# Performance work log

Hardware: AMD Instinct MI355X
Metric: run time of the kernel (lower is better)

## Reference

```python
import jax, jax.numpy as jnp
import numpy as np

DIM = 512
BLOCK = 64
SPARSITY = 0.9
B, L = 4, 2048
NEG_INF = jnp.float32(-jnp.inf)


def _block_sparse_mask(key, seq_len, block_size, sparsity):
    # mirrors BasicQuantumAttention._get_block_sparse_mask, with diagonal
    # blocks forced on so no softmax row is fully masked (avoids NaNs)
    nb = (seq_len + block_size - 1) // block_size
    blk = jax.random.uniform(key, (nb, nb)) > sparsity
    blk = jnp.tril(blk) | jnp.eye(nb, dtype=bool)
    m = jnp.repeat(jnp.repeat(blk, block_size, axis=0), block_size, axis=1)
    return m[:seq_len, :seq_len]


def setup_inputs() -> dict:
    key = jax.random.key(0)
    ks = jax.random.split(key, 12)
    d = DIM
    inp = {}
    names = ['q_real', 'q_imag', 'k_real', 'k_imag', 'v_real', 'v_imag']
    for i, n in enumerate(names):
        inp[n] = jax.random.normal(ks[i], (B, L, d), dtype=jnp.float32)
    # xavier-ish init for Linear weights (torch Linear: y = x @ W.T + b)
    s6 = (2.0 / (6 * d + 6 * d)) ** 0.5
    s2 = (2.0 / (2 * d + 2 * d)) ** 0.5
    inp['W_qkv'] = jax.random.normal(ks[6], (6 * d, 6 * d), dtype=jnp.float32) * s6
    inp['b_qkv'] = jnp.zeros((6 * d,), dtype=jnp.float32)
    inp['W_out'] = jax.random.normal(ks[7], (2 * d, 2 * d), dtype=jnp.float32) * s2
    inp['b_out'] = jnp.zeros((2 * d,), dtype=jnp.float32)
    # two independent random block-sparse masks (one per stream, as in the
    # original which regenerates the mask inside each _chunk_attention call)
    inp['mask_real'] = _block_sparse_mask(ks[8], L, BLOCK, SPARSITY)
    inp['mask_imag'] = _block_sparse_mask(ks[9], L, BLOCK, SPARSITY)
    return inp


def _masked_attention(q, k, v, mask, scale):
    # q,k,v: [B,L,d]; mask: [L,L] bool (True = keep)
    scores = jnp.einsum('bqd,bkd->bqk', q, k) * scale
    scores = jnp.where(mask[None, :, :], scores, NEG_INF)
    attn = jax.nn.softmax(scores, axis=-1)  # dropout is identity in eval
    return jnp.einsum('bqk,bkd->bqd', attn, v)


def reference(q_real, q_imag, k_real, k_imag, v_real, v_imag,
              W_qkv, b_qkv, W_out, b_out, mask_real, mask_imag):
    d = q_real.shape[-1]
    scale = jnp.asarray(d, q_real.dtype) ** -0.5
    x = jnp.concatenate([q_real, q_imag, k_real, k_imag, v_real, v_imag], axis=-1)
    qkv = x @ W_qkv.T + b_qkv                       # [B,L,6d]
    q_r, q_i, k_r, k_i, v_r, v_i = jnp.split(qkv, 6, axis=-1)
    out_real = _masked_attention(q_r, k_r, v_r, mask_real, scale)
    out_imag = _masked_attention(q_i, k_i, v_i, mask_imag, scale)
    out = jnp.concatenate([out_real, out_imag], axis=-1)  # [B,L,2d]
    out = out @ W_out.T + b_out
    return out[..., :d], out[..., d:]
```

## Files before the change

### kernel.cpp

```cpp
#include <hip/hip_runtime.h>
#include <stdint.h>

typedef __attribute__((ext_vector_type(8))) short short8;
typedef __attribute__((ext_vector_type(4))) float f32x4;

#define DEV __device__ __forceinline__

DEV unsigned short f2bf(float f) {
    unsigned int u = __float_as_uint(f);
    u += 0x7FFFu + ((u >> 16) & 1u);
    return (unsigned short)(u >> 16);
}

DEV void gload_lds16(const void* g, void* l) {
    __builtin_amdgcn_global_load_lds(
        (const __attribute__((address_space(1))) unsigned int*)g,
        (__attribute__((address_space(3))) unsigned int*)l,
        16, 0, 0);
}

__global__ __launch_bounds__(256) void f32_to_bf16_k(
    const float* __restrict__ in, unsigned short* __restrict__ out, int n8) {
    int i = blockIdx.x * 256 + threadIdx.x;
    if (i >= n8) return;
    const float4* src = (const float4*)in + (size_t)i * 2;
    float4 a = src[0], b = src[1];
    short8 o;
    o[0] = f2bf(a.x); o[1] = f2bf(a.y); o[2] = f2bf(a.z); o[3] = f2bf(a.w);
    o[4] = f2bf(b.x); o[5] = f2bf(b.y); o[6] = f2bf(b.z); o[7] = f2bf(b.w);
    *((short8*)out + i) = o;
}

__global__ __launch_bounds__(256) void pack_x_k(
    const float* __restrict__ p0, const float* __restrict__ p1,
    const float* __restrict__ p2, const float* __restrict__ p3,
    const float* __restrict__ p4, const float* __restrict__ p5,
    unsigned short* __restrict__ x) {
    int i = blockIdx.x * 256 + threadIdx.x;
    int e0 = i * 8;
    int m = e0 / 3072;
    int k = e0 - m * 3072;
    int sel = k >> 9;
    const float* src;
    switch (sel) {
        case 0: src = p0; break; case 1: src = p1; break;
        case 2: src = p2; break; case 3: src = p3; break;
        case 4: src = p4; break; default: src = p5; break;
    }
    src += (size_t)m * 512 + (k & 511);
    float4 a = *(const float4*)src;
    float4 b = *(const float4*)(src + 4);
    short8 o;
    o[0] = f2bf(a.x); o[1] = f2bf(a.y); o[2] = f2bf(a.z); o[3] = f2bf(a.w);
    o[4] = f2bf(b.x); o[5] = f2bf(b.y); o[6] = f2bf(b.z); o[7] = f2bf(b.w);
    *(short8*)(x + e0) = o;
}

__global__ void scan_masks_k(const void* mr, const void* mi,
                             int* __restrict__ nact, unsigned char* __restrict__ lists) {
    int t = threadIdx.x;
    if (t >= 64) return;
    int s = t >> 5, qb = t & 31;
    const unsigned char* det = (const unsigned char*)mr;
    bool is_byte = det[1] != 0;
    const void* m = s ? mi : mr;
    int cnt = 0;
    for (int kb = 0; kb < 32; ++kb) {
        size_t off = (size_t)(qb * 64) * 2048 + (size_t)kb * 64;
        bool on = is_byte ? (((const unsigned char*)m)[off] != 0)
                          : (((const int*)m)[off] != 0);
        if (on) lists[t * 32 + cnt++] = (unsigned char)kb;
    }
    nact[t] = cnt;
}


#define MFMA16(mbase)                                                          \
    do {                                                                       \
        _Pragma("unroll")                                                      \
        for (int m_ = 0; m_ < 4; ++m_) {                                       \
            _Pragma("unroll")                                                  \
            for (int n_ = 0; n_ < 4; ++n_)                                     \
                acc[(mbase) + m_][n_] = __builtin_amdgcn_mfma_f32_16x16x32_bf16( \
                    af[m_], bf[n_], acc[(mbase) + m_][n_], 0, 0, 0);           \
        }                                                                      \
    } while (0)

#define PHASE_PRE()                                          \
    __builtin_amdgcn_s_barrier();                            \
    asm volatile("s_waitcnt lgkmcnt(0)" ::: "memory");       \
    __builtin_amdgcn_sched_barrier(0);                       \
    __builtin_amdgcn_s_setprio(1)

#define PHASE_END()                                          \
    __builtin_amdgcn_s_setprio(0);                           \
    __builtin_amdgcn_s_barrier();                            \
    asm volatile("" ::: "memory")

#define PHASE_END_V4()                                       \
    __builtin_amdgcn_s_setprio(0);                           \
    asm volatile("s_waitcnt vmcnt(4)" ::: "memory");         \
    __builtin_amdgcn_s_barrier();                            \
    asm volatile("" ::: "memory")

template <int MODE>
__global__ __launch_bounds__(512, 2) void gemm256(
    const unsigned short* __restrict__ A, const unsigned short* __restrict__ B,
    const float* __restrict__ bias, unsigned short* __restrict__ Cb,
    float* __restrict__ Cf, int M, int N, int K, int NBN, int halfN, int half_elems) {
    __shared__ unsigned short lds[2][4][8192];
    const int tid = threadIdx.x;
    const int wv = tid >> 6, ln = tid & 63;
    const int fr = ln & 15, fo = ln >> 4;
    const int wr = wv >> 2, wc = wv & 3;
    const int cpx = gridDim.x >> 3;
    const int wgid = (blockIdx.x & 7) * cpx + (blockIdx.x >> 3);
    const int bm = wgid / NBN, bn = wgid % NBN;
    const unsigned short* Abase = A + (size_t)(bm * 256) * K;
    const unsigned short* Bbase = B + (size_t)(bn * 256) * K;
    const int NT = K >> 6;
    const int NI = NT >> 1;

    auto stagePair = [&](int buf, int isB, int t) {
        const unsigned short* G = isB ? Bbase : Abase;
        unsigned short* Ld = &lds[buf][isB ? 2 : 0][0];
        const int kcol = t * 64;
        #pragma unroll
        for (int r2 = 0; r2 < 4; ++r2) {
            int d = r2 * 8192 + wv * 1024 + ln * 16;
            int s = d ^ (((d >> 7) & 7) << 4);
            int grow = s >> 7;
            int gcol = (s & 127) >> 1;
            gload_lds16(G + (size_t)grow * K + kcol + gcol,
                        (char*)Ld + r2 * 8192 + wv * 1024);
        }
    };
    auto readA = [&](int buf, int mh, int ks, short8* dst) {
        #pragma unroll
        for (int m = 0; m < 4; ++m) {
            int row = wr * 128 + mh * 64 + m * 16 + fr;
            int byte = (row * 128 + ks * 64 + fo * 16) ^ ((row & 7) << 4);
            dst[m] = *(const short8*)((const char*)&lds[buf][0][0] + byte);
        }
    };
    auto readB = [&](int buf, int ks, short8* dst) {
        #pragma unroll
        for (int n = 0; n < 4; ++n) {
            int row = wc * 64 + n * 16 + fr;
            int byte = (row * 128 + ks * 64 + fo * 16) ^ ((row & 7) << 4);
            dst[n] = *(const short8*)((const char*)&lds[buf][2][0] + byte);
        }
    };

    f32x4 acc[8][4];
    #pragma unroll
    for (int m = 0; m < 8; ++m)
        #pragma unroll
        for (int n = 0; n < 4; ++n) acc[m][n] = f32x4{0.f, 0.f, 0.f, 0.f};

    stagePair(0, 0, 0);
    stagePair(0, 1, 0);
    stagePair(1, 1, 1);
    asm volatile("s_waitcnt vmcnt(4)" ::: "memory");
    __builtin_amdgcn_s_barrier();
    asm volatile("" ::: "memory");

    for (int i = 0; i < NI; ++i) {
        const int t1 = 2 * i + 1;
        const int tn0 = (2 * i + 2) % NT;
        const int tn1 = (2 * i + 3) % NT;
        short8 af[4], bf[4];
        readA(0, 0, 0, af); readB(0, 0, bf);
        stagePair(1, 0, t1);
        PHASE_PRE(); MFMA16(0); PHASE_END();
        readA(0, 1, 0, af);
        PHASE_PRE(); MFMA16(4); PHASE_END();
        readA(0, 0, 1, af); readB(0, 1, bf);
        PHASE_PRE(); MFMA16(0); PHASE_END();
        readA(0, 1, 1, af);
        stagePair(0, 1, tn0);
        PHASE_PRE(); MFMA16(4); PHASE_END_V4();
        readA(1, 0, 0, af); readB(1, 0, bf);
        stagePair(0, 0, tn0);
        PHASE_PRE(); MFMA16(0); PHASE_END();
        readA(1, 1, 0, af);
        PHASE_PRE(); MFMA16(4); PHASE_END();
        readA(1, 0, 1, af); readB(1, 1, bf);
        PHASE_PRE(); MFMA16(0); PHASE_END();
        readA(1, 1, 1, af);
        stagePair(1, 1, tn1);
        PHASE_PRE(); MFMA16(4); PHASE_END_V4();
    }

    #pragma unroll
    for (int mi = 0; mi < 8; ++mi)
        #pragma unroll
        for (int ni = 0; ni < 4; ++ni)
            #pragma unroll
            for (int j = 0; j < 4; ++j) {
                int gr = bm * 256 + wr * 128 + mi * 16 + fo * 4 + j;
                int gc = bn * 256 + wc * 64 + ni * 16 + fr;
                float v = acc[mi][ni][j] + bias[gc];
                if (MODE == 0) {
                    Cb[(size_t)gr * N + gc] = f2bf(v);
                } else {
                    if (gc < halfN) Cf[(size_t)gr * halfN + gc] = v;
                    else Cf[half_elems + (size_t)gr * halfN + (gc - halfN)] = v;
                }
            }
}

__global__ __launch_bounds__(256) void transpose_v_k(
    const unsigned short* __restrict__ qkv, unsigned short* __restrict__ Vt) {
    int idx = blockIdx.x;
    int kt = idx & 31; idx >>= 5;
    int dt = idx & 7;  idx >>= 3;
    int b  = idx & 3;  idx >>= 2;
    int s  = idx;
    __shared__ unsigned short tile[64][65];
    int t = threadIdx.x;
    int r = t >> 2;
    int cs = (t & 3) * 16;
    const unsigned short* src =
        qkv + (size_t)(b * 2048 + kt * 64 + r) * 3072 + 2048 + s * 512 + dt * 64 + cs;
    short8 v0 = *(const short8*)src;
    short8 v1 = *(const short8*)(src + 8);
    #pragma unroll
    for (int i = 0; i < 8; ++i) { tile[r][cs + i] = v0[i]; tile[r][cs + 8 + i] = v1[i]; }
    __syncthreads();
    short8 o0, o1;
    #pragma unroll
    for (int i = 0; i < 8; ++i) { o0[i] = tile[cs + i][r]; o1[i] = tile[cs + 8 + i][r]; }
    unsigned short* dst =
        Vt + (size_t)((s * 4 + b) * 512 + dt * 64 + r) * 2048 + kt * 64 + cs;
    *(short8*)dst = o0;
    *(short8*)(dst + 8) = o1;
}

__global__ __launch_bounds__(64) void attn_k(
    const unsigned short* __restrict__ qkv, const unsigned short* __restrict__ Vt,
    unsigned short* __restrict__ attn, const int* __restrict__ nact,
    const unsigned char* __restrict__ lists) {
    int wg = blockIdx.x;
    int xcd = wg & 7, idx = wg >> 3;
    int b = xcd >> 1, s = xcd & 1;
    int qb = idx >> 2, quarter = idx & 3;
    int lane = threadIdx.x;
    int fr = lane & 15, fo = lane >> 4;
    const float scale = 0.04419417382415922f;
    __shared__ unsigned short Pl[1024];
    unsigned char* Plb = (unsigned char*)&Pl[0];

    int qoff = s * 512, koff = 1024 + s * 512;
    size_t vtbase = (size_t)((s * 4 + b) * 512) * 2048;
    int mrow = b * 2048 + qb * 64 + quarter * 16;

    short8 qf[16];
    const unsigned short* qrow_ptr = qkv + (size_t)(mrow + fr) * 3072 + qoff + fo * 8;
    #pragma unroll
    for (int kk = 0; kk < 16; ++kk) qf[kk] = *(const short8*)(qrow_ptr + kk * 32);

    f32x4 acc[32];
    #pragma unroll
    for (int di = 0; di < 32; ++di) acc[di] = f32x4{0.f, 0.f, 0.f, 0.f};
    float mr[4] = {-1e30f, -1e30f, -1e30f, -1e30f};
    float lr[4] = {0.f, 0.f, 0.f, 0.f};

    int na = nact[s * 32 + qb];
    const unsigned char* lst = lists + (s * 32 + qb) * 32;

    for (int t = 0; t < na; ++t) {
        int kb = lst[t];
        const unsigned short* kbase_ptr =
            qkv + (size_t)(b * 2048 + kb * 64 + fr) * 3072 + koff + fo * 8;
        f32x4 sf[4];
        #pragma unroll
        for (int nf = 0; nf < 4; ++nf) {
            sf[nf] = f32x4{0.f, 0.f, 0.f, 0.f};
            const unsigned short* kp = kbase_ptr + (size_t)nf * 16 * 3072;
            #pragma unroll
            for (int kk = 0; kk < 16; ++kk) {
                short8 kf = *(const short8*)(kp + kk * 32);
                sf[nf] = __builtin_amdgcn_mfma_f32_16x16x32_bf16(qf[kk], kf, sf[nf], 0, 0, 0);
            }
        }
        #pragma unroll
        for (int nf = 0; nf < 4; ++nf) sf[nf] *= scale;
        float bm[4], f_[4], rs[4];
        #pragma unroll
        for (int j = 0; j < 4; ++j) {
            float v = fmaxf(fmaxf(sf[0][j], sf[1][j]), fmaxf(sf[2][j], sf[3][j]));
            #pragma unroll
            for (int off = 1; off < 16; off <<= 1) v = fmaxf(v, __shfl_xor(v, off, 64));
            bm[j] = v;
        }
        #pragma unroll
        for (int j = 0; j < 4; ++j) {
            float mn = fmaxf(mr[j], bm[j]);
            f_[j] = __expf(mr[j] - mn);
            mr[j] = mn;
            rs[j] = 0.f;
        }
        #pragma unroll
        for (int nf = 0; nf < 4; ++nf)
            #pragma unroll
            for (int j = 0; j < 4; ++j) {
                float p = __expf(sf[nf][j] - mr[j]);
                sf[nf][j] = p;
                rs[j] += p;
            }
        #pragma unroll
        for (int j = 0; j < 4; ++j) {
            float v = rs[j];
            #pragma unroll
            for (int off = 1; off < 16; off <<= 1) v += __shfl_xor(v, off, 64);
            lr[j] = lr[j] * f_[j] + v;
        }
        #pragma unroll
        for (int di = 0; di < 32; ++di) {
            acc[di][0] *= f_[0]; acc[di][1] *= f_[1];
            acc[di][2] *= f_[2]; acc[di][3] *= f_[3];
        }
        #pragma unroll
        for (int nf = 0; nf < 4; ++nf)
            #pragma unroll
            for (int j = 0; j < 4; ++j) {
                int row = fo * 4 + j, col = nf * 16 + fr;
                int byte = row * 128 + ((col * 2) ^ ((row & 7) << 4));
                *(unsigned short*)(Plb + byte) = f2bf(sf[nf][j]);
            }
        asm volatile("s_waitcnt lgkmcnt(0)" ::: "memory");
        #pragma unroll
        for (int ks = 0; ks < 2; ++ks) {
            int rbyte = fr * 128 + (((ks * 32 + fo * 8) * 2) ^ ((fr & 7) << 4));
            short8 pf = *(const short8*)(Plb + rbyte);
            const unsigned short* vp =
                Vt + vtbase + (size_t)fr * 2048 + kb * 64 + ks * 32 + fo * 8;
            #pragma unroll
            for (int di = 0; di < 32; ++di) {
                short8 vf = *(const short8*)(vp + (size_t)di * 16 * 2048);
                acc[di] = __builtin_amdgcn_mfma_f32_16x16x32_bf16(pf, vf, acc[di], 0, 0, 0);
            }
        }
    }
    float inv[4];
    #pragma unroll
    for (int j = 0; j < 4; ++j) inv[j] = 1.0f / lr[j];
    unsigned short* orow = attn + (size_t)(mrow + fo * 4) * 1024 + s * 512 + fr;
    #pragma unroll
    for (int di = 0; di < 32; ++di)
        #pragma unroll
        for (int j = 0; j < 4; ++j)
            orow[(size_t)j * 1024 + di * 16] = f2bf(acc[di][j] * inv[j]);
}

extern "C" void kernel_launch(void* const* d_in, const int* in_sizes, int n_in,
                              void* d_out, int out_size, void* d_ws, size_t ws_size,
                              hipStream_t stream) {
    const float* q_r = (const float*)d_in[0];
    const float* q_i = (const float*)d_in[1];
    const float* k_r = (const float*)d_in[2];
    const float* k_i = (const float*)d_in[3];
    const float* v_r = (const float*)d_in[4];
    const float* v_i = (const float*)d_in[5];
    const float* W_qkv = (const float*)d_in[6];
    const float* b_qkv = (const float*)d_in[7];
    const float* W_out = (const float*)d_in[8];
    const float* b_out = (const float*)d_in[9];
    const void* mask_r = d_in[10];
    const void* mask_i = d_in[11];

    char* ws = (char*)d_ws;
    unsigned short* x    = (unsigned short*)(ws);
    unsigned short* Wq   = (unsigned short*)(ws + 50331648);
    unsigned short* qkv  = (unsigned short*)(ws + 69206016);
    unsigned short* Wo   = (unsigned short*)(ws + 119537664);
    int* nact            = (int*)(ws + 121634816);
    unsigned char* lists = (unsigned char*)(ws + 121634816 + 256);
    unsigned short* Vt   = x;
    unsigned short* attn = x + 8388608;

    f32_to_bf16_k<<<4608, 256, 0, stream>>>(W_qkv, Wq, 1179648);
    f32_to_bf16_k<<<512, 256, 0, stream>>>(W_out, Wo, 131072);
    pack_x_k<<<12288, 256, 0, stream>>>(q_r, q_i, k_r, k_i, v_r, v_i, x);
    scan_masks_k<<<1, 64, 0, stream>>>(mask_r, mask_i, nact, lists);
    gemm256<0><<<384, 512, 0, stream>>>(x, Wq, b_qkv, qkv, nullptr,
                                        8192, 3072, 3072, 12, 0, 0);
    transpose_v_k<<<2048, 256, 0, stream>>>(qkv, Vt);
    attn_k<<<1024, 64, 0, stream>>>(qkv, Vt, attn, nact, lists);
    gemm256<1><<<128, 512, 0, stream>>>(attn, Wo, b_out, nullptr, (float*)d_out,
                                        8192, 1024, 1024, 4, 512, 4194304);
}
```

Baseline: 531.4 us.

## Retile QKV GEMM to 256x192, split attention head dim, parallelize mask scan

The QKV projection GEMM is templated on the N-tile width and launched with 256x192 tiles, giving 512 workgroups instead of 384 for a better fit to the CU count. The attention kernel splits the 512-wide head dimension into two halves per workgroup, doubling the grid to 2048 and halving accumulator registers so two waves can fit per SIMD. The cost is that QK^T is recomputed once per half. The mask scan now uses one block per query block with a ballot and popcount compaction instead of a single serial thread loop, and the K-fragment loads are interleaved across the four score tiles.

```diff
diff --git a/kernel.cpp b/kernel.cpp
--- a/kernel.cpp
+++ b/kernel.cpp
@@ -58,29 +58,33 @@
 
 __global__ void scan_masks_k(const void* mr, const void* mi,
                              int* __restrict__ nact, unsigned char* __restrict__ lists) {
-    int t = threadIdx.x;
-    if (t >= 64) return;
-    int s = t >> 5, qb = t & 31;
+    int blk = blockIdx.x;
+    int s = blk >> 5, qb = blk & 31;
+    int lane = threadIdx.x;
     const unsigned char* det = (const unsigned char*)mr;
     bool is_byte = det[1] != 0;
     const void* m = s ? mi : mr;
-    int cnt = 0;
-    for (int kb = 0; kb < 32; ++kb) {
-        size_t off = (size_t)(qb * 64) * 2048 + (size_t)kb * 64;
-        bool on = is_byte ? (((const unsigned char*)m)[off] != 0)
-                          : (((const int*)m)[off] != 0);
-        if (on) lists[t * 32 + cnt++] = (unsigned char)kb;
+    bool on = false;
+    if (lane < 32) {
+        size_t off = (size_t)(qb * 64) * 2048 + (size_t)lane * 64;
+        on = is_byte ? (((const unsigned char*)m)[off] != 0)
+                     : (((const int*)m)[off] != 0);
     }
-    nact[t] = cnt;
-}
-
-
-#define MFMA16(mbase)                                                          \
+    unsigned long long mask = __ballot(on);
+    if (on) {
+        int pos = __popcll(mask & ((1ull << lane) - 1ull));
+        lists[blk * 32 + pos] = (unsigned char)lane;
+    }
+    if (lane == 0) nact[blk] = (int)__popcll(mask);
+}
+
+
+#define MFMA_TILE(mbase)                                                       \
     do {                                                                       \
         _Pragma("unroll")                                                      \
         for (int m_ = 0; m_ < 4; ++m_) {                                       \
             _Pragma("unroll")                                                  \
-            for (int n_ = 0; n_ < 4; ++n_)                                     \
+            for (int n_ = 0; n_ < NF; ++n_)                                    \
                 acc[(mbase) + m_][n_] = __builtin_amdgcn_mfma_f32_16x16x32_bf16( \
                     af[m_], bf[n_], acc[(mbase) + m_][n_], 0, 0, 0);           \
         }                                                                      \
@@ -97,18 +101,25 @@
     __builtin_amdgcn_s_barrier();                            \
     asm volatile("" ::: "memory")
 
-#define PHASE_END_V4()                                       \
+#define WAIT_VN()                                                          \
+    do {                                                                   \
+        if constexpr (NF == 3) asm volatile("s_waitcnt vmcnt(3)" ::: "memory"); \
+        else asm volatile("s_waitcnt vmcnt(4)" ::: "memory");              \
+    } while (0)
+
+#define PHASE_END_VN()                                       \
     __builtin_amdgcn_s_setprio(0);                           \
-    asm volatile("s_waitcnt vmcnt(4)" ::: "memory");         \
+    WAIT_VN();                                               \
     __builtin_amdgcn_s_barrier();                            \
     asm volatile("" ::: "memory")
 
-template <int MODE>
+template <int MODE, int NF>
 __global__ __launch_bounds__(512, 2) void gemm256(
     const unsigned short* __restrict__ A, const unsigned short* __restrict__ B,
     const float* __restrict__ bias, unsigned short* __restrict__ Cb,
     float* __restrict__ Cf, int M, int N, int K, int NBN, int halfN, int half_elems) {
-    __shared__ unsigned short lds[2][4][8192];
+    constexpr int BN = NF * 64;
+    __shared__ unsigned short lds[2][16384 + NF * 4096];
     const int tid = threadIdx.x;
     const int wv = tid >> 6, ln = tid & 63;
     const int fr = ln & 15, fo = ln >> 4;
@@ -117,20 +128,21 @@
     const int wgid = (blockIdx.x & 7) * cpx + (blockIdx.x >> 3);
     const int bm = wgid / NBN, bn = wgid % NBN;
     const unsigned short* Abase = A + (size_t)(bm * 256) * K;
-    const unsigned short* Bbase = B + (size_t)(bn * 256) * K;
+    const unsigned short* Bbase = B + (size_t)(bn * BN) * K;
     const int NT = K >> 6;
     const int NI = NT >> 1;
 
     auto stagePair = [&](int buf, int isB, int t) {
         const unsigned short* G = isB ? Bbase : Abase;
-        unsigned short* Ld = &lds[buf][isB ? 2 : 0][0];
+        unsigned short* Ld = &lds[buf][isB ? 16384 : 0];
         const int kcol = t * 64;
-        #pragma unroll
-        for (int r2 = 0; r2 < 4; ++r2) {
+        const int nch = isB ? NF : 4;
+        #pragma unroll
+        for (int r2 = 0; r2 < nch; ++r2) {
             int d = r2 * 8192 + wv * 1024 + ln * 16;
-            int s = d ^ (((d >> 7) & 7) << 4);
-            int grow = s >> 7;
-            int gcol = (s & 127) >> 1;
+            int sw = d ^ (((d >> 7) & 7) << 4);
+            int grow = sw >> 7;
+            int gcol = (sw & 127) >> 1;
             gload_lds16(G + (size_t)grow * K + kcol + gcol,
                         (char*)Ld + r2 * 8192 + wv * 1024);
         }
@@ -140,28 +152,28 @@
         for (int m = 0; m < 4; ++m) {
             int row = wr * 128 + mh * 64 + m * 16 + fr;
             int byte = (row * 128 + ks * 64 + fo * 16) ^ ((row & 7) << 4);
-            dst[m] = *(const short8*)((const char*)&lds[buf][0][0] + byte);
+            dst[m] = *(const short8*)((const char*)&lds[buf][0] + byte);
         }
     };
     auto readB = [&](int buf, int ks, short8* dst) {
         #pragma unroll
-        for (int n = 0; n < 4; ++n) {
-            int row = wc * 64 + n * 16 + fr;
+        for (int n = 0; n < NF; ++n) {
+            int row = wc * (NF * 16) + n * 16 + fr;
             int byte = (row * 128 + ks * 64 + fo * 16) ^ ((row & 7) << 4);
-            dst[n] = *(const short8*)((const char*)&lds[buf][2][0] + byte);
+            dst[n] = *(const short8*)((const char*)&lds[buf][16384] + byte);
         }
     };
 
-    f32x4 acc[8][4];
+    f32x4 acc[8][NF];
     #pragma unroll
     for (int m = 0; m < 8; ++m)
         #pragma unroll
-        for (int n = 0; n < 4; ++n) acc[m][n] = f32x4{0.f, 0.f, 0.f, 0.f};
+        for (int n = 0; n < NF; ++n) acc[m][n] = f32x4{0.f, 0.f, 0.f, 0.f};
 
     stagePair(0, 0, 0);
     stagePair(0, 1, 0);
     stagePair(1, 1, 1);
-    asm volatile("s_waitcnt vmcnt(4)" ::: "memory");
+    WAIT_VN();
     __builtin_amdgcn_s_barrier();
     asm volatile("" ::: "memory");
 
@@ -172,34 +184,34 @@
         short8 af[4], bf[4];
         readA(0, 0, 0, af); readB(0, 0, bf);
         stagePair(1, 0, t1);
-        PHASE_PRE(); MFMA16(0); PHASE_END();
+        PHASE_PRE(); MFMA_TILE(0); PHASE_END();
         readA(0, 1, 0, af);
-        PHASE_PRE(); MFMA16(4); PHASE_END();
+        PHASE_PRE(); MFMA_TILE(4); PHASE_END();
         readA(0, 0, 1, af); readB(0, 1, bf);
-        PHASE_PRE(); MFMA16(0); PHASE_END();
+        PHASE_PRE(); MFMA_TILE(0); PHASE_END();
         readA(0, 1, 1, af);
         stagePair(0, 1, tn0);
-        PHASE_PRE(); MFMA16(4); PHASE_END_V4();
+        PHASE_PRE(); MFMA_TILE(4); PHASE_END_VN();
         readA(1, 0, 0, af); readB(1, 0, bf);
         stagePair(0, 0, tn0);
-        PHASE_PRE(); MFMA16(0); PHASE_END();
+        PHASE_PRE(); MFMA_TILE(0); PHASE_END();
         readA(1, 1, 0, af);
-        PHASE_PRE(); MFMA16(4); PHASE_END();
+        PHASE_PRE(); MFMA_TILE(4); PHASE_END();
         readA(1, 0, 1, af); readB(1, 1, bf);
-        PHASE_PRE(); MFMA16(0); PHASE_END();
+        PHASE_PRE(); MFMA_TILE(0); PHASE_END();
         readA(1, 1, 1, af);
         stagePair(1, 1, tn1);
-        PHASE_PRE(); MFMA16(4); PHASE_END_V4();
+        PHASE_PRE(); MFMA_TILE(4); PHASE_END_VN();
     }
 
     #pragma unroll
     for (int mi = 0; mi < 8; ++mi)
         #pragma unroll
-        for (int ni = 0; ni < 4; ++ni)
+        for (int ni = 0; ni < NF; ++ni)
             #pragma unroll
             for (int j = 0; j < 4; ++j) {
                 int gr = bm * 256 + wr * 128 + mi * 16 + fo * 4 + j;
-                int gc = bn * 256 + wc * 64 + ni * 16 + fr;
+                int gc = bn * BN + wc * (NF * 16) + ni * 16 + fr;
                 float v = acc[mi][ni][j] + bias[gc];
                 if (MODE == 0) {
                     Cb[(size_t)gr * N + gc] = f2bf(v);
@@ -237,14 +249,14 @@
     *(short8*)(dst + 8) = o1;
 }
 
-__global__ __launch_bounds__(64) void attn_k(
+__global__ __launch_bounds__(64, 2) void attn_k(
     const unsigned short* __restrict__ qkv, const unsigned short* __restrict__ Vt,
     unsigned short* __restrict__ attn, const int* __restrict__ nact,
     const unsigned char* __restrict__ lists) {
     int wg = blockIdx.x;
     int xcd = wg & 7, idx = wg >> 3;
     int b = xcd >> 1, s = xcd & 1;
-    int qb = idx >> 2, quarter = idx & 3;
+    int qb = idx >> 3, quarter = (idx >> 1) & 3, dh = idx & 1;
     int lane = threadIdx.x;
     int fr = lane & 15, fo = lane >> 4;
     const float scale = 0.04419417382415922f;
@@ -252,7 +264,7 @@
     unsigned char* Plb = (unsigned char*)&Pl[0];
 
     int qoff = s * 512, koff = 1024 + s * 512;
-    size_t vtbase = (size_t)((s * 4 + b) * 512) * 2048;
+    size_t vtbase = (size_t)((s * 4 + b) * 512 + dh * 256) * 2048;
     int mrow = b * 2048 + qb * 64 + quarter * 16;
 
     short8 qf[16];
@@ -260,9 +272,9 @@
     #pragma unroll
     for (int kk = 0; kk < 16; ++kk) qf[kk] = *(const short8*)(qrow_ptr + kk * 32);
 
-    f32x4 acc[32];
-    #pragma unroll
-    for (int di = 0; di < 32; ++di) acc[di] = f32x4{0.f, 0.f, 0.f, 0.f};
+    f32x4 acc[16];
+    #pragma unroll
+    for (int di = 0; di < 16; ++di) acc[di] = f32x4{0.f, 0.f, 0.f, 0.f};
     float mr[4] = {-1e30f, -1e30f, -1e30f, -1e30f};
     float lr[4] = {0.f, 0.f, 0.f, 0.f};
 
@@ -271,18 +283,21 @@
 
     for (int t = 0; t < na; ++t) {
         int kb = lst[t];
-        const unsigned short* kbase_ptr =
+        const unsigned short* kbp =
             qkv + (size_t)(b * 2048 + kb * 64 + fr) * 3072 + koff + fo * 8;
         f32x4 sf[4];
         #pragma unroll
-        for (int nf = 0; nf < 4; ++nf) {
-            sf[nf] = f32x4{0.f, 0.f, 0.f, 0.f};
-            const unsigned short* kp = kbase_ptr + (size_t)nf * 16 * 3072;
-            #pragma unroll
-            for (int kk = 0; kk < 16; ++kk) {
-                short8 kf = *(const short8*)(kp + kk * 32);
-                sf[nf] = __builtin_amdgcn_mfma_f32_16x16x32_bf16(qf[kk], kf, sf[nf], 0, 0, 0);
-            }
+        for (int nf = 0; nf < 4; ++nf) sf[nf] = f32x4{0.f, 0.f, 0.f, 0.f};
+        #pragma unroll 4
+        for (int kk = 0; kk < 16; ++kk) {
+            short8 k0 = *(const short8*)(kbp + kk * 32);
+            short8 k1 = *(const short8*)(kbp + (size_t)16 * 3072 + kk * 32);
+            short8 k2 = *(const short8*)(kbp + (size_t)32 * 3072 + kk * 32);
+            short8 k3 = *(const short8*)(kbp + (size_t)48 * 3072 + kk * 32);
+            sf[0] = __builtin_amdgcn_mfma_f32_16x16x32_bf16(qf[kk], k0, sf[0], 0, 0, 0);
+            sf[1] = __builtin_amdgcn_mfma_f32_16x16x32_bf16(qf[kk], k1, sf[1], 0, 0, 0);
+            sf[2] = __builtin_amdgcn_mfma_f32_16x16x32_bf16(qf[kk], k2, sf[2], 0, 0, 0);
+            sf[3] = __builtin_amdgcn_mfma_f32_16x16x32_bf16(qf[kk], k3, sf[3], 0, 0, 0);
         }
         #pragma unroll
         for (int nf = 0; nf < 4; ++nf) sf[nf] *= scale;
@@ -317,7 +332,7 @@
             lr[j] = lr[j] * f_[j] + v;
         }
         #pragma unroll
-        for (int di = 0; di < 32; ++di) {
+        for (int di = 0; di < 16; ++di) {
             acc[di][0] *= f_[0]; acc[di][1] *= f_[1];
             acc[di][2] *= f_[2]; acc[di][3] *= f_[3];
         }
@@ -336,8 +351,8 @@
             short8 pf = *(const short8*)(Plb + rbyte);
             const unsigned short* vp =
                 Vt + vtbase + (size_t)fr * 2048 + kb * 64 + ks * 32 + fo * 8;
-            #pragma unroll
-            for (int di = 0; di < 32; ++di) {
+            #pragma unroll 4
+            for (int di = 0; di < 16; ++di) {
                 short8 vf = *(const short8*)(vp + (size_t)di * 16 * 2048);
                 acc[di] = __builtin_amdgcn_mfma_f32_16x16x32_bf16(pf, vf, acc[di], 0, 0, 0);
             }
@@ -346,9 +361,9 @@
     float inv[4];
     #pragma unroll
     for (int j = 0; j < 4; ++j) inv[j] = 1.0f / lr[j];
-    unsigned short* orow = attn + (size_t)(mrow + fo * 4) * 1024 + s * 512 + fr;
-    #pragma unroll
-    for (int di = 0; di < 32; ++di)
+    unsigned short* orow = attn + (size_t)(mrow + fo * 4) * 1024 + s * 512 + dh * 256 + fr;
+    #pragma unroll
+    for (int di = 0; di < 16; ++di)
         #pragma unroll
         for (int j = 0; j < 4; ++j)
             orow[(size_t)j * 1024 + di * 16] = f2bf(acc[di][j] * inv[j]);
@@ -383,11 +398,11 @@
     f32_to_bf16_k<<<4608, 256, 0, stream>>>(W_qkv, Wq, 1179648);
     f32_to_bf16_k<<<512, 256, 0, stream>>>(W_out, Wo, 131072);
     pack_x_k<<<12288, 256, 0, stream>>>(q_r, q_i, k_r, k_i, v_r, v_i, x);
-    scan_masks_k<<<1, 64, 0, stream>>>(mask_r, mask_i, nact, lists);
-    gemm256<0><<<384, 512, 0, stream>>>(x, Wq, b_qkv, qkv, nullptr,
-                                        8192, 3072, 3072, 12, 0, 0);
+    scan_masks_k<<<64, 64, 0, stream>>>(mask_r, mask_i, nact, lists);
+    gemm256<0, 3><<<512, 512, 0, stream>>>(x, Wq, b_qkv, qkv, nullptr,
+                                           8192, 3072, 3072, 16, 0, 0);
     transpose_v_k<<<2048, 256, 0, stream>>>(qkv, Vt);
-    attn_k<<<1024, 64, 0, stream>>>(qkv, Vt, attn, nact, lists);
-    gemm256<1><<<128, 512, 0, stream>>>(attn, Wo, b_out, nullptr, (float*)d_out,
-                                        8192, 1024, 1024, 4, 512, 4194304);
-}
+    attn_k<<<2048, 64, 0, stream>>>(qkv, Vt, attn, nact, lists);
+    gemm256<1, 4><<<128, 512, 0, stream>>>(attn, Wo, b_out, nullptr, (float*)d_out,
+                                           8192, 1024, 1024, 4, 512, 4194304);
+}
```

New measurement: 592.4 us. 1.11x slower.
